# Optimization experiments

Measured on AMD Instinct MI355X. Metric: run time of the kernel, lower is better.

Reference implementation:

```python
import jax, jax.numpy as jnp
import numpy as np

T, B, N_IN, N_RNN, N_OUT = 1000, 128, 85, 512, 33
ALPHA = 0.2
SIGMA = float(np.sqrt(2.0 / ALPHA) * 0.05)  # sqrt(2/alpha) * sigma_rec


def setup_inputs() -> dict:
    key = jax.random.key(0)
    k_x, k_win, k_wout, k_noise = jax.random.split(key, 4)
    x = jax.random.normal(k_x, (T, B, N_IN), dtype=jnp.float32)
    # weight = concat(w_in0, w_rec0) along axis 0, per LeakyRNNCell init
    w_in0 = jax.random.normal(k_win, (N_IN, N_RNN), dtype=jnp.float32) / np.sqrt(N_IN)  # _w_in_start=1.0
    w_rec0 = 0.5 * jnp.eye(N_RNN, dtype=jnp.float32)  # 'diag' init, _w_rec_start=0.5 (softplus)
    W = jnp.concatenate([w_in0, w_rec0], axis=0)  # [N_IN+N_RNN, N_RNN]
    b = jnp.zeros((N_RNN,), dtype=jnp.float32)
    W_out = jax.random.normal(k_wout, (N_RNN, N_OUT), dtype=jnp.float32) / np.sqrt(N_RNN)
    b_out = jnp.zeros((N_OUT,), dtype=jnp.float32)
    # recurrent noise randn_like(state)*sigma, precomputed for all timesteps
    noise = jax.random.normal(k_noise, (T, B, N_RNN), dtype=jnp.float32) * SIGMA
    return {"x": x, "W": W, "b": b, "W_out": W_out, "b_out": b_out, "noise": noise}


def reference(x, W, b, W_out, b_out, noise):
    # Leaky RNN: h_t = (1-alpha)*h_{t-1} + alpha*softplus([x_t, h_{t-1}] @ W + b + noise_t)
    def step(state, xs):
        x_t, n_t = xs
        gate = jnp.concatenate([x_t, state], axis=1) @ W + b + n_t  # [B, N_RNN]
        out = (1.0 - ALPHA) * state + ALPHA * jax.nn.softplus(gate)
        return out, out

    state0 = jnp.zeros((x.shape[1], W.shape[1]), dtype=x.dtype)
    _, h = jax.lax.scan(step, state0, (x, noise))  # h: [T, B, N_RNN]
    y_hat = jax.nn.sigmoid(h @ W_out + b_out)  # lsq loss head: [T, B, N_OUT]
    return y_hat, h
```

## Files before the change

### kernel.cpp

```cpp
#include <hip/hip_runtime.h>
#include <cmath>

#define T_STEPS 1000
#define B_SZ    128
#define N_IN    85
#define N_RNN   512
#define N_OUT   33
#define K_PAD   88
#define Y_SIZE  (T_STEPS * B_SZ * N_OUT)

__global__ void k_zero_flag(int* flag) {
    if (threadIdx.x == 0 && blockIdx.x == 0) *flag = 0;
}

__global__ void k_check_diag(const float* __restrict__ W, int* flag) {
    const float* Wr = W + N_IN * N_RNN;
    bool bad = false;
    for (int i = blockIdx.x * blockDim.x + threadIdx.x;
         i < N_RNN * N_RNN; i += gridDim.x * blockDim.x) {
        int r = i >> 9, c = i & (N_RNN - 1);
        float v = Wr[i];
        if (r != c && v != 0.0f) bad = true;
    }
    if (bad) atomicOr(flag, 1);
}

__device__ __forceinline__ float softplus_f(float g) {
    return fmaxf(g, 0.0f) + __logf(1.0f + __expf(-fabsf(g)));
}

__global__ __launch_bounds__(128) void k_scan_fused(
        const float* __restrict__ x, const float* __restrict__ W,
        const float* __restrict__ bias, const float* __restrict__ noise,
        float* __restrict__ H, const int* __restrict__ flag) {
    if (*flag != 0) return;
    const int tid = threadIdx.x;
    const int b   = blockIdx.x >> 2;
    const int n   = ((blockIdx.x & 3) << 7) + tid;

    float wcol[K_PAD];
    #pragma unroll
    for (int k = 0; k < N_IN; ++k) wcol[k] = W[k * N_RNN + n];
    wcol[85] = 0.f; wcol[86] = 0.f; wcol[87] = 0.f;
    const float dn = W[(N_IN + n) * N_RNN + n];
    const float bn = bias[n];

    __shared__ __align__(16) float xs[2][8][K_PAD];
    const int row = tid >> 4;
    const int l16 = tid & 15;

    const size_t strT = (size_t)B_SZ * N_RNN;
    const float* np = noise + (size_t)b * N_RNN + n;
    float*       hp = H     + (size_t)b * N_RNN + n;

    float rA[8], rB[8], xr[6];
    float h = 0.0f;

    auto XLD = [&](int t0) {
        const int t = t0 + row;
        const float* xrow = x + ((size_t)t * B_SZ + b) * N_IN;
        #pragma unroll
        for (int j = 0; j < 6; ++j) {
            const int k = l16 + 16 * j;
            xr[j] = (t < T_STEPS && k < N_IN) ? xrow[k] : 0.0f;
        }
    };
    auto XST = [&](int buf) {
        #pragma unroll
        for (int j = 0; j < 6; ++j) {
            const int k = l16 + 16 * j;
            if (k < K_PAD) xs[buf][row][k] = xr[j];
        }
    };
    auto pref8 = [&](float (&ring)[8], int t0) {
        #pragma unroll
        for (int u = 0; u < 8; ++u) ring[u] = np[(size_t)(t0 + u) * strT];
    };
    auto consume8 = [&](float (&ring)[8], int t0, int buf) {
        #pragma unroll
        for (int u = 0; u < 8; ++u) {
            const float4* xv4 = (const float4*)(&xs[buf][u][0]);
            float a0 = 0.f, a1 = 0.f, a2 = 0.f, a3 = 0.f;
            #pragma unroll
            for (int k4 = 0; k4 < K_PAD / 4; ++k4) {
                const float4 xv = xv4[k4];
                a0 = fmaf(xv.x, wcol[4 * k4 + 0], a0);
                a1 = fmaf(xv.y, wcol[4 * k4 + 1], a1);
                a2 = fmaf(xv.z, wcol[4 * k4 + 2], a2);
                a3 = fmaf(xv.w, wcol[4 * k4 + 3], a3);
            }
            const float g = ((a0 + a1) + (a2 + a3)) + (bn + ring[u]) + dn * h;
            h = 0.8f * h + 0.2f * softplus_f(g);
            hp[(size_t)(t0 + u) * strT] = h;
        }
    };

    pref8(rA, 0);
    XLD(0); XST(0);
    XLD(8);
    asm volatile("s_waitcnt lgkmcnt(0)" ::: "memory");
    __builtin_amdgcn_s_barrier();
    __builtin_amdgcn_sched_barrier(0);

    int cur = 0;
    #pragma unroll 1
    for (int tb2 = 0; tb2 < 62; ++tb2) {
        const int bb = tb2 << 1;
        pref8(rB, (bb + 1) << 3);
        consume8(rA, bb << 3, cur);
        XST(cur ^ 1);
        XLD((bb + 2) << 3);
        asm volatile("s_waitcnt lgkmcnt(0)" ::: "memory");
        __builtin_amdgcn_s_barrier();
        __builtin_amdgcn_sched_barrier(0);
        cur ^= 1;
        pref8(rA, (bb + 2) << 3);
        consume8(rB, (bb + 1) << 3, cur);
        XST(cur ^ 1);
        XLD((bb + 3) << 3);
        asm volatile("s_waitcnt lgkmcnt(0)" ::: "memory");
        __builtin_amdgcn_s_barrier();
        __builtin_amdgcn_sched_barrier(0);
        cur ^= 1;
    }
    consume8(rA, 992, cur);
}

__global__ __launch_bounds__(256) void k_precompute(
        const float* __restrict__ x, const float* __restrict__ W,
        const float* __restrict__ bias, const float* __restrict__ noise,
        float* __restrict__ G, const int* __restrict__ flag) {
    if (*flag == 0) return;
    __shared__ float xsh[128 * K_PAD];
    const int tid = threadIdx.x;
    const int n   = ((blockIdx.x & 1) << 8) + tid;
    const int r0  = (blockIdx.x >> 1) << 7;

    float wcol[K_PAD];
    #pragma unroll
    for (int k = 0; k < N_IN; ++k) wcol[k] = W[k * N_RNN + n];
    wcol[85] = 0.f; wcol[86] = 0.f; wcol[87] = 0.f;

    const float* xsrc = x + (size_t)r0 * N_IN;
    for (int i = tid; i < 128 * K_PAD; i += 256) {
        const int r = i / K_PAD;
        const int k = i - r * K_PAD;
        xsh[i] = (k < N_IN) ? xsrc[r * N_IN + k] : 0.0f;
    }
    const float bn = bias[n];
    __syncthreads();

    for (int rb = 0; rb < 16; ++rb) {
        const int rbase = rb << 3;
        const size_t gbase = (size_t)(r0 + rbase) * N_RNN + n;
        float npv[8];
        #pragma unroll
        for (int rr = 0; rr < 8; ++rr) npv[rr] = noise[gbase + (size_t)rr * N_RNN];
        float acc[8] = {0.f, 0.f, 0.f, 0.f, 0.f, 0.f, 0.f, 0.f};
        #pragma unroll
        for (int k4 = 0; k4 < K_PAD / 4; ++k4) {
            const float w0 = wcol[4 * k4 + 0];
            const float w1 = wcol[4 * k4 + 1];
            const float w2 = wcol[4 * k4 + 2];
            const float w3 = wcol[4 * k4 + 3];
            #pragma unroll
            for (int rr = 0; rr < 8; ++rr) {
                const float4 xv = *(const float4*)&xsh[(rbase + rr) * K_PAD + 4 * k4];
                acc[rr] = fmaf(xv.x, w0, acc[rr]);
                acc[rr] = fmaf(xv.y, w1, acc[rr]);
                acc[rr] = fmaf(xv.z, w2, acc[rr]);
                acc[rr] = fmaf(xv.w, w3, acc[rr]);
            }
        }
        #pragma unroll
        for (int rr = 0; rr < 8; ++rr) {
            G[gbase + (size_t)rr * N_RNN] = acc[rr] + bn + npv[rr];
        }
    }
}

__global__ __launch_bounds__(512) void k_scan_general(const float* __restrict__ W,
                                                      float* __restrict__ GH,
                                                      const int* __restrict__ flag) {
    if (*flag == 0) return;
    const int b = blockIdx.x;
    const int n = threadIdx.x;
    const int strideT = B_SZ * N_RNN;
    float* base = GH + b * N_RNN + n;
    float h = 0.0f;
    __shared__ float hs[N_RNN];
    const float* Wr = W + N_IN * N_RNN;
    for (int t = 0; t < T_STEPS; ++t) {
        hs[n] = h;
        __syncthreads();
        float g = base[t * strideT];
        for (int k = 0; k < N_RNN; ++k) {
            g = fmaf(hs[k], Wr[k * N_RNN + n], g);
        }
        const float sp = softplus_f(g);
        h = 0.8f * h + 0.2f * sp;
        base[t * strideT] = h;
        __syncthreads();
    }
}

__global__ __launch_bounds__(256) void k_head(const float* __restrict__ hbase,
                                              const float* __restrict__ Wout,
                                              const float* __restrict__ bout,
                                              float* __restrict__ y) {
    __shared__ float ws[N_RNN][36];
    __shared__ float bs[64];
    const int tid = threadIdx.x;
    for (int i = tid; i < N_RNN * N_OUT; i += 256) {
        int k = i / N_OUT;
        int o = i - k * N_OUT;
        ws[k][o] = Wout[i];
    }
    if (tid < N_OUT) bs[tid] = bout[tid];
    __syncthreads();

    const int row = blockIdx.x * 256 + tid;
    const float* hr = hbase + (size_t)row * N_RNN;
    float acc[N_OUT];
    #pragma unroll
    for (int o = 0; o < N_OUT; ++o) acc[o] = bs[o];

    for (int k4 = 0; k4 < N_RNN / 4; ++k4) {
        const float4 hv = *(const float4*)(hr + 4 * k4);
        const float* w0 = &ws[4 * k4][0];
        #pragma unroll
        for (int j = 0; j < 4; ++j) {
            const float hx = (j == 0) ? hv.x : (j == 1) ? hv.y : (j == 2) ? hv.z : hv.w;
            const float4* wr = (const float4*)(w0 + j * 36);
            #pragma unroll
            for (int oo = 0; oo < 8; ++oo) {
                const float4 wv = wr[oo];
                acc[4 * oo + 0] = fmaf(hx, wv.x, acc[4 * oo + 0]);
                acc[4 * oo + 1] = fmaf(hx, wv.y, acc[4 * oo + 1]);
                acc[4 * oo + 2] = fmaf(hx, wv.z, acc[4 * oo + 2]);
                acc[4 * oo + 3] = fmaf(hx, wv.w, acc[4 * oo + 3]);
            }
            acc[32] = fmaf(hx, w0[j * 36 + 32], acc[32]);
        }
    }
    float* yr = y + (size_t)row * N_OUT;
    #pragma unroll
    for (int o = 0; o < N_OUT; ++o) {
        yr[o] = 1.0f / (1.0f + __expf(-acc[o]));
    }
}

extern "C" void kernel_launch(void* const* d_in, const int* in_sizes, int n_in,
                              void* d_out, int out_size, void* d_ws, size_t ws_size,
                              hipStream_t stream) {
    const float* x     = (const float*)d_in[0];
    const float* W     = (const float*)d_in[1];
    const float* bias  = (const float*)d_in[2];
    const float* Wout  = (const float*)d_in[3];
    const float* bout  = (const float*)d_in[4];
    const float* noise = (const float*)d_in[5];

    float* y  = (float*)d_out;
    float* GH = y + Y_SIZE;
    int* flag = (int*)d_out;

    k_zero_flag<<<1, 64, 0, stream>>>(flag);
    k_check_diag<<<256, 256, 0, stream>>>(W, flag);
    k_scan_fused<<<512, 128, 0, stream>>>(x, W, bias, noise, GH, flag);
    k_precompute<<<2000, 256, 0, stream>>>(x, W, bias, noise, GH, flag);
    k_scan_general<<<128, 512, 0, stream>>>(W, GH, flag);
    k_head<<<500, 256, 0, stream>>>(GH, Wout, bout, y);
}
```

Before: 997.5 us.

## Shrink scan blocks to single wavefronts handling two columns, drop barriers, register-block head

The fused scan kernel now runs one 64-thread wavefront per block, with each thread computing two hidden columns. Because the block is a single wave, the LDS x-tile exchange no longer needs s_barrier, which removes a per-8-step synchronisation at the cost of doubled register pressure and half as many threads in flight. The x loader clamps t instead of predicating. The head kernel now has each thread compute four rows against shared W_out to reuse LDS reads, which raises register use to about 132 accumulators per thread and lowers occupancy.

```diff
diff --git a/kernel.cpp b/kernel.cpp
--- a/kernel.cpp
+++ b/kernel.cpp
@@ -29,101 +29,115 @@
     return fmaxf(g, 0.0f) + __logf(1.0f + __expf(-fabsf(g)));
 }
 
-__global__ __launch_bounds__(128) void k_scan_fused(
+__global__ __launch_bounds__(64, 1) void k_scan_fused(
         const float* __restrict__ x, const float* __restrict__ W,
         const float* __restrict__ bias, const float* __restrict__ noise,
         float* __restrict__ H, const int* __restrict__ flag) {
     if (*flag != 0) return;
     const int tid = threadIdx.x;
     const int b   = blockIdx.x >> 2;
-    const int n   = ((blockIdx.x & 3) << 7) + tid;
-
-    float wcol[K_PAD];
+    const int q   = blockIdx.x & 3;
+    const int n0  = (q << 7) + tid;
+    const int n1  = n0 + 64;
+
+    float w0[K_PAD], w1[K_PAD];
     #pragma unroll
-    for (int k = 0; k < N_IN; ++k) wcol[k] = W[k * N_RNN + n];
-    wcol[85] = 0.f; wcol[86] = 0.f; wcol[87] = 0.f;
-    const float dn = W[(N_IN + n) * N_RNN + n];
-    const float bn = bias[n];
+    for (int k = 0; k < N_IN; ++k) {
+        w0[k] = W[k * N_RNN + n0];
+        w1[k] = W[k * N_RNN + n1];
+    }
+    w0[85] = w0[86] = w0[87] = 0.f;
+    w1[85] = w1[86] = w1[87] = 0.f;
+    const float d0 = W[(N_IN + n0) * N_RNN + n0];
+    const float d1 = W[(N_IN + n1) * N_RNN + n1];
+    const float b0 = bias[n0];
+    const float b1 = bias[n1];
 
     __shared__ __align__(16) float xs[2][8][K_PAD];
-    const int row = tid >> 4;
-    const int l16 = tid & 15;
+    const int row = tid >> 3;
+    const int l8  = tid & 7;
 
     const size_t strT = (size_t)B_SZ * N_RNN;
-    const float* np = noise + (size_t)b * N_RNN + n;
-    float*       hp = H     + (size_t)b * N_RNN + n;
-
-    float rA[8], rB[8], xr[6];
-    float h = 0.0f;
+    const float* npA = noise + (size_t)b * N_RNN + n0;
+    const float* npB = npA + 64;
+    float*       hpA = H     + (size_t)b * N_RNN + n0;
+    float*       hpB = hpA + 64;
+
+    float rA0[8], rA1[8], rB0[8], rB1[8], xr[11];
+    float h0 = 0.0f, h1 = 0.0f;
 
     auto XLD = [&](int t0) {
-        const int t = t0 + row;
+        int t = t0 + row;
+        if (t > T_STEPS - 1) t = T_STEPS - 1;
         const float* xrow = x + ((size_t)t * B_SZ + b) * N_IN;
         #pragma unroll
-        for (int j = 0; j < 6; ++j) {
-            const int k = l16 + 16 * j;
-            xr[j] = (t < T_STEPS && k < N_IN) ? xrow[k] : 0.0f;
-        }
+        for (int j = 0; j < 10; ++j) xr[j] = xrow[l8 + 8 * j];
+        xr[10] = (l8 < 5) ? xrow[80 + l8] : 0.0f;
     };
     auto XST = [&](int buf) {
         #pragma unroll
-        for (int j = 0; j < 6; ++j) {
-            const int k = l16 + 16 * j;
-            if (k < K_PAD) xs[buf][row][k] = xr[j];
-        }
+        for (int j = 0; j < 11; ++j) xs[buf][row][l8 + 8 * j] = xr[j];
     };
-    auto pref8 = [&](float (&ring)[8], int t0) {
-        #pragma unroll
-        for (int u = 0; u < 8; ++u) ring[u] = np[(size_t)(t0 + u) * strT];
+    auto pref8 = [&](float (&r0)[8], float (&r1)[8], int t0) {
+        #pragma unroll
+        for (int u = 0; u < 8; ++u) {
+            r0[u] = npA[(size_t)(t0 + u) * strT];
+            r1[u] = npB[(size_t)(t0 + u) * strT];
+        }
     };
-    auto consume8 = [&](float (&ring)[8], int t0, int buf) {
+    auto consume8 = [&](float (&r0)[8], float (&r1)[8], int t0, int buf) {
         #pragma unroll
         for (int u = 0; u < 8; ++u) {
             const float4* xv4 = (const float4*)(&xs[buf][u][0]);
             float a0 = 0.f, a1 = 0.f, a2 = 0.f, a3 = 0.f;
+            float c0 = 0.f, c1 = 0.f, c2 = 0.f, c3 = 0.f;
             #pragma unroll
             for (int k4 = 0; k4 < K_PAD / 4; ++k4) {
                 const float4 xv = xv4[k4];
-                a0 = fmaf(xv.x, wcol[4 * k4 + 0], a0);
-                a1 = fmaf(xv.y, wcol[4 * k4 + 1], a1);
-                a2 = fmaf(xv.z, wcol[4 * k4 + 2], a2);
-                a3 = fmaf(xv.w, wcol[4 * k4 + 3], a3);
+                a0 = fmaf(xv.x, w0[4 * k4 + 0], a0);
+                a1 = fmaf(xv.y, w0[4 * k4 + 1], a1);
+                a2 = fmaf(xv.z, w0[4 * k4 + 2], a2);
+                a3 = fmaf(xv.w, w0[4 * k4 + 3], a3);
+                c0 = fmaf(xv.x, w1[4 * k4 + 0], c0);
+                c1 = fmaf(xv.y, w1[4 * k4 + 1], c1);
+                c2 = fmaf(xv.z, w1[4 * k4 + 2], c2);
+                c3 = fmaf(xv.w, w1[4 * k4 + 3], c3);
             }
-            const float g = ((a0 + a1) + (a2 + a3)) + (bn + ring[u]) + dn * h;
-            h = 0.8f * h + 0.2f * softplus_f(g);
-            hp[(size_t)(t0 + u) * strT] = h;
+            const float g0 = ((a0 + a1) + (a2 + a3)) + (b0 + r0[u]) + d0 * h0;
+            const float g1 = ((c0 + c1) + (c2 + c3)) + (b1 + r1[u]) + d1 * h1;
+            h0 = 0.8f * h0 + 0.2f * softplus_f(g0);
+            h1 = 0.8f * h1 + 0.2f * softplus_f(g1);
+            hpA[(size_t)(t0 + u) * strT] = h0;
+            hpB[(size_t)(t0 + u) * strT] = h1;
         }
     };
 
-    pref8(rA, 0);
+    pref8(rA0, rA1, 0);
     XLD(0); XST(0);
     XLD(8);
     asm volatile("s_waitcnt lgkmcnt(0)" ::: "memory");
-    __builtin_amdgcn_s_barrier();
     __builtin_amdgcn_sched_barrier(0);
 
     int cur = 0;
     #pragma unroll 1
     for (int tb2 = 0; tb2 < 62; ++tb2) {
         const int bb = tb2 << 1;
-        pref8(rB, (bb + 1) << 3);
-        consume8(rA, bb << 3, cur);
+        pref8(rB0, rB1, (bb + 1) << 3);
+        consume8(rA0, rA1, bb << 3, cur);
         XST(cur ^ 1);
         XLD((bb + 2) << 3);
         asm volatile("s_waitcnt lgkmcnt(0)" ::: "memory");
-        __builtin_amdgcn_s_barrier();
         __builtin_amdgcn_sched_barrier(0);
         cur ^= 1;
-        pref8(rA, (bb + 2) << 3);
-        consume8(rB, (bb + 1) << 3, cur);
+        pref8(rA0, rA1, (bb + 2) << 3);
+        consume8(rB0, rB1, (bb + 1) << 3, cur);
         XST(cur ^ 1);
         XLD((bb + 3) << 3);
         asm volatile("s_waitcnt lgkmcnt(0)" ::: "memory");
-        __builtin_amdgcn_s_barrier();
         __builtin_amdgcn_sched_barrier(0);
         cur ^= 1;
     }
-    consume8(rA, 992, cur);
+    consume8(rA0, rA1, 992, cur);
 }
 
 __global__ __launch_bounds__(256) void k_precompute(
@@ -204,14 +218,14 @@
     }
 }
 
-__global__ __launch_bounds__(256) void k_head(const float* __restrict__ hbase,
-                                              const float* __restrict__ Wout,
-                                              const float* __restrict__ bout,
-                                              float* __restrict__ y) {
+__global__ __launch_bounds__(128, 1) void k_head(const float* __restrict__ hbase,
+                                                 const float* __restrict__ Wout,
+                                                 const float* __restrict__ bout,
+                                                 float* __restrict__ y) {
     __shared__ float ws[N_RNN][36];
     __shared__ float bs[64];
     const int tid = threadIdx.x;
-    for (int i = tid; i < N_RNN * N_OUT; i += 256) {
+    for (int i = tid; i < N_RNN * N_OUT; i += 128) {
         int k = i / N_OUT;
         int o = i - k * N_OUT;
         ws[k][o] = Wout[i];
@@ -219,34 +233,69 @@
     if (tid < N_OUT) bs[tid] = bout[tid];
     __syncthreads();
 
-    const int row = blockIdx.x * 256 + tid;
-    const float* hr = hbase + (size_t)row * N_RNN;
-    float acc[N_OUT];
+    const int wid  = (blockIdx.x << 1) + (tid >> 6);
+    const int lane = tid & 63;
+    const int base = (wid << 8) + lane;
+
+    const float* hr0 = hbase + (size_t)base * N_RNN;
+    const float* hr1 = hr0 + (size_t)64 * N_RNN;
+    const float* hr2 = hr0 + (size_t)128 * N_RNN;
+    const float* hr3 = hr0 + (size_t)192 * N_RNN;
+
+    float acc[4][N_OUT];
     #pragma unroll
-    for (int o = 0; o < N_OUT; ++o) acc[o] = bs[o];
+    for (int o = 0; o < N_OUT; ++o) {
+        const float bo = bs[o];
+        acc[0][o] = bo; acc[1][o] = bo; acc[2][o] = bo; acc[3][o] = bo;
+    }
 
     for (int k4 = 0; k4 < N_RNN / 4; ++k4) {
-        const float4 hv = *(const float4*)(hr + 4 * k4);
-        const float* w0 = &ws[4 * k4][0];
+        const float4 hv0 = *(const float4*)(hr0 + 4 * k4);
+        const float4 hv1 = *(const float4*)(hr1 + 4 * k4);
+        const float4 hv2 = *(const float4*)(hr2 + 4 * k4);
+        const float4 hv3 = *(const float4*)(hr3 + 4 * k4);
         #pragma unroll
         for (int j = 0; j < 4; ++j) {
-            const float hx = (j == 0) ? hv.x : (j == 1) ? hv.y : (j == 2) ? hv.z : hv.w;
-            const float4* wr = (const float4*)(w0 + j * 36);
+            const float hx0 = ((const float*)&hv0)[j];
+            const float hx1 = ((const float*)&hv1)[j];
+            const float hx2 = ((const float*)&hv2)[j];
+            const float hx3 = ((const float*)&hv3)[j];
+            const float* wj = &ws[4 * k4 + j][0];
+            const float4* wr = (const float4*)wj;
             #pragma unroll
             for (int oo = 0; oo < 8; ++oo) {
                 const float4 wv = wr[oo];
-                acc[4 * oo + 0] = fmaf(hx, wv.x, acc[4 * oo + 0]);
-                acc[4 * oo + 1] = fmaf(hx, wv.y, acc[4 * oo + 1]);
-                acc[4 * oo + 2] = fmaf(hx, wv.z, acc[4 * oo + 2]);
-                acc[4 * oo + 3] = fmaf(hx, wv.w, acc[4 * oo + 3]);
+                acc[0][4 * oo + 0] = fmaf(hx0, wv.x, acc[0][4 * oo + 0]);
+                acc[0][4 * oo + 1] = fmaf(hx0, wv.y, acc[0][4 * oo + 1]);
+                acc[0][4 * oo + 2] = fmaf(hx0, wv.z, acc[0][4 * oo + 2]);
+                acc[0][4 * oo + 3] = fmaf(hx0, wv.w, acc[0][4 * oo + 3]);
+                acc[1][4 * oo + 0] = fmaf(hx1, wv.x, acc[1][4 * oo + 0]);
+                acc[1][4 * oo + 1] = fmaf(hx1, wv.y, acc[1][4 * oo + 1]);
+                acc[1][4 * oo + 2] = fmaf(hx1, wv.z, acc[1][4 * oo + 2]);
+                acc[1][4 * oo + 3] = fmaf(hx1, wv.w, acc[1][4 * oo + 3]);
+                acc[2][4 * oo + 0] = fmaf(hx2, wv.x, acc[2][4 * oo + 0]);
+                acc[2][4 * oo + 1] = fmaf(hx2, wv.y, acc[2][4 * oo + 1]);
+                acc[2][4 * oo + 2] = fmaf(hx2, wv.z, acc[2][4 * oo + 2]);
+                acc[2][4 * oo + 3] = fmaf(hx2, wv.w, acc[2][4 * oo + 3]);
+                acc[3][4 * oo + 0] = fmaf(hx3, wv.x, acc[3][4 * oo + 0]);
+                acc[3][4 * oo + 1] = fmaf(hx3, wv.y, acc[3][4 * oo + 1]);
+                acc[3][4 * oo + 2] = fmaf(hx3, wv.z, acc[3][4 * oo + 2]);
+                acc[3][4 * oo + 3] = fmaf(hx3, wv.w, acc[3][4 * oo + 3]);
             }
-            acc[32] = fmaf(hx, w0[j * 36 + 32], acc[32]);
-        }
-    }
-    float* yr = y + (size_t)row * N_OUT;
+            const float w32 = wj[32];
+            acc[0][32] = fmaf(hx0, w32, acc[0][32]);
+            acc[1][32] = fmaf(hx1, w32, acc[1][32]);
+            acc[2][32] = fmaf(hx2, w32, acc[2][32]);
+            acc[3][32] = fmaf(hx3, w32, acc[3][32]);
+        }
+    }
     #pragma unroll
-    for (int o = 0; o < N_OUT; ++o) {
-        yr[o] = 1.0f / (1.0f + __expf(-acc[o]));
+    for (int i = 0; i < 4; ++i) {
+        float* yr = y + (size_t)(base + 64 * i) * N_OUT;
+        #pragma unroll
+        for (int o = 0; o < N_OUT; ++o) {
+            yr[o] = 1.0f / (1.0f + __expf(-acc[i][o]));
+        }
     }
 }
 
@@ -266,8 +315,8 @@
 
     k_zero_flag<<<1, 64, 0, stream>>>(flag);
     k_check_diag<<<256, 256, 0, stream>>>(W, flag);
-    k_scan_fused<<<512, 128, 0, stream>>>(x, W, bias, noise, GH, flag);
+    k_scan_fused<<<512, 64, 0, stream>>>(x, W, bias, noise, GH, flag);
     k_precompute<<<2000, 256, 0, stream>>>(x, W, bias, noise, GH, flag);
     k_scan_general<<<128, 512, 0, stream>>>(W, GH, flag);
-    k_head<<<500, 256, 0, stream>>>(GH, Wout, bout, y);
-}
+    k_head<<<250, 128, 0, stream>>>(GH, Wout, bout, y);
+}
```

After: 1.215 ms. 1.22x slower.
